# Kernel optimization log

Hardware: AMD Instinct MI355X
Metric: run time of the kernel (lower is better)

The kernel has to match this reference:

```python
import jax, jax.numpy as jnp
import numpy as np

N_NODES = 50000
IN_CH = 128
OUT_CH = 64
HID = 2 * OUT_CH  # 128
N_EDGES = 800000


def _glorot(key, shape):
    fan_in, fan_out = shape[0], shape[-1]
    lim = jnp.sqrt(6.0 / (fan_in + fan_out))
    return jax.random.uniform(key, shape, jnp.float32, -lim, lim)


def setup_inputs() -> dict:
    key = jax.random.key(0)
    ks = jax.random.split(key, 10)
    x = jax.random.normal(ks[0], (N_NODES, IN_CH), jnp.float32)
    edge_index = jax.random.randint(ks[1], (2, N_EDGES), 0, N_NODES, jnp.int32)
    return {
        "x": x,
        "edge_index": edge_index,
        "W1": _glorot(ks[2], (IN_CH, HID)),
        "a_src1": _glorot(ks[3], (HID,)),
        "a_dst1": _glorot(ks[4], (HID,)),
        "b1": jnp.zeros((HID,), jnp.float32),
        "W2": _glorot(ks[5], (HID, OUT_CH)),
        "a_src2": _glorot(ks[6], (OUT_CH,)),
        "a_dst2": _glorot(ks[7], (OUT_CH,)),
        "b2": jnp.zeros((OUT_CH,), jnp.float32),
    }


def _gat_conv(x, src, dst, W, a_src, a_dst, b, n_nodes):
    # Linear transform: [N, F_out]
    h = x @ W
    # Per-node attention halves (heads=1): alpha_i = <h_i, a>
    al_s = h @ a_src  # [N]
    al_d = h @ a_dst  # [N]
    # Edge scores with LeakyReLU(0.2), PyG default negative slope
    e = jax.nn.leaky_relu(al_s[src] + al_d[dst], negative_slope=0.2)
    # Segment softmax over incoming edges of each dst node
    m = jax.ops.segment_max(e, dst, num_segments=n_nodes)
    m = jnp.where(jnp.isfinite(m), m, 0.0)
    ex = jnp.exp(e - m[dst])
    denom = jax.ops.segment_sum(ex, dst, num_segments=n_nodes)
    alpha = ex / (denom[dst] + 1e-16)  # [E]
    # Weighted scatter-add aggregation
    out = jax.ops.segment_sum(h[src] * alpha[:, None], dst, num_segments=n_nodes)
    return out + b


def reference(x, edge_index, W1, a_src1, a_dst1, b1, W2, a_src2, a_dst2, b2):
    n = x.shape[0]
    # add_self_loops=True (PyG GATConv default)
    loops = jnp.arange(n, dtype=edge_index.dtype)
    src = jnp.concatenate([edge_index[0], loops])
    dst = jnp.concatenate([edge_index[1], loops])
    h = _gat_conv(x.astype(jnp.float32), src, dst, W1, a_src1, a_dst1, b1, n)
    h = jax.nn.relu(h)
    return _gat_conv(h, src, dst, W2, a_src2, a_dst2, b2, n)
```

## Files before the change

### kernel.cpp

```cpp
#include <hip/hip_runtime.h>
#include <hip/hip_bf16.h>

#define N_NODES 50000
#define IN_CH 128
#define HID 128
#define OUT_CH 64
#define N_EDGES 800000
#define N_TOT_EDGES (N_EDGES + N_NODES)
#define ET_PAD (N_TOT_EDGES + 3 * N_NODES)
#define MPAD 50048
#define NBN ((N_NODES + 255) / 256)
#define NB_E ((N_EDGES + 255) / 256)
#define NB_ET ((N_TOT_EDGES + 255) / 256)
#define NB_GEMM (MPAD / 64)

typedef float float4v __attribute__((ext_vector_type(4)));
typedef unsigned uint4v __attribute__((ext_vector_type(4)));
typedef __attribute__((ext_vector_type(8))) short bf16x8;
typedef __attribute__((ext_vector_type(4))) float f32x4;

__device__ __forceinline__ unsigned bf16_rne(float f) {
    unsigned u = __float_as_uint(f);
    return (u + 0x7fffu + ((u >> 16) & 1u)) >> 16;
}
__device__ __forceinline__ unsigned pack2(float a, float b) {
    return bf16_rne(a) | (bf16_rne(b) << 16);
}

__global__ __launch_bounds__(256) void k_pre(
        int* __restrict__ cnt,
        const float* __restrict__ W1, unsigned short* __restrict__ Wl1,
        const float* __restrict__ W2, unsigned short* __restrict__ Wl2, int n) {
    const int b = blockIdx.x, t = threadIdx.x;
    if (b < NBN) {
        int i = b * 256 + t;
        if (i < n) cnt[i] = 1;
        return;
    }
    const float* W; unsigned short* Wl; int N, bb;
    if (b < NBN + 8) { W = W1; Wl = Wl1; N = 128; bb = b - NBN; }
    else             { W = W2; Wl = Wl2; N = 64;  bb = b - NBN - 8; }
    const int tg = bb * 256 + t;
    if (tg >= 16 * N) return;
    const int kg = tg / N, col = tg & (N - 1);
    float v[8];
    #pragma unroll
    for (int j = 0; j < 8; ++j) v[j] = W[(size_t)(kg * 8 + j) * N + col];
    uint4 p;
    p.x = pack2(v[0], v[1]); p.y = pack2(v[2], v[3]);
    p.z = pack2(v[4], v[5]); p.w = pack2(v[6], v[7]);
    *(uint4*)&Wl[(size_t)tg * 8] = p;
}


__device__ __forceinline__ void count_body(int b, int t,
        const int* __restrict__ dst_row, int* __restrict__ cnt,
        unsigned short* __restrict__ rank, int e) {
    int i = b * 256 + t;
    if (i < e) {
        int d = __builtin_nontemporal_load(&dst_row[i]);
        rank[i] = (unsigned short)atomicAdd(&cnt[d], 1);
    }
}

template<int N, bool AF32>
__device__ __forceinline__ void gemm_body(int gb, int t,
        const float* __restrict__ Xf, const unsigned short* __restrict__ Xb,
        const unsigned short* __restrict__ Wlg,
        const float* __restrict__ asrc, const float* __restrict__ adst,
        unsigned short* __restrict__ Hb, float* __restrict__ als,
        float* __restrict__ ald, int M, unsigned short* Wl) {
    constexpr int NF = N / 16;
    for (int i = t; i < N * 16; i += 256)
        ((uint4*)Wl)[i] = ((const uint4*)Wlg)[i];
    __syncthreads();

    const int lane = t & 63, w = t >> 6;
    const int rb = gb * 64 + w * 16;
    const int cl = lane & 15, g = lane >> 4;

    f32x4 acc[NF];
    #pragma unroll
    for (int n = 0; n < NF; ++n) acc[n] = (f32x4){0.f, 0.f, 0.f, 0.f};

    const float* Xrow = nullptr;
    const unsigned short* Abase = nullptr;
    if constexpr (AF32) {
        const int arow = (rb + cl < M) ? (rb + cl) : (M - 1);
        Xrow = Xf + (size_t)arow * 128;
    } else {
        Abase = Xb + (size_t)(rb >> 4) * 2048 + cl * 8;
    }

    #pragma unroll
    for (int s = 0; s < 4; ++s) {
        bf16x8 af;
        if constexpr (AF32) {
            const int k0 = (s * 4 + g) * 8;
            float4 a = *(const float4*)&Xrow[k0];
            float4 c = *(const float4*)&Xrow[k0 + 4];
            uint4v uu;
            uu[0] = pack2(a.x, a.y); uu[1] = pack2(a.z, a.w);
            uu[2] = pack2(c.x, c.y); uu[3] = pack2(c.z, c.w);
            af = __builtin_bit_cast(bf16x8, uu);
        } else {
            af = *(const bf16x8*)(Abase + (s * 4 + g) * 128);
        }
        #pragma unroll
        for (int n = 0; n < NF; ++n) {
            bf16x8 bf = *(const bf16x8*)(Wl + ((s * 4 + g) * N + n * 16 + cl) * 8);
            acc[n] = __builtin_amdgcn_mfma_f32_16x16x32_bf16(af, bf, acc[n], 0, 0, 0);
        }
    }

    float asv[NF], adv[NF];
    #pragma unroll
    for (int n = 0; n < NF; ++n) {
        asv[n] = asrc[n * 16 + cl];
        adv[n] = adst[n * 16 + cl];
    }

    #pragma unroll
    for (int r = 0; r < 4; ++r) {
        float ps = 0.f, pd = 0.f;
        #pragma unroll
        for (int n = 0; n < NF; ++n) {
            ps += acc[n][r] * asv[n];
            pd += acc[n][r] * adv[n];
        }
        #pragma unroll
        for (int mask = 1; mask < 16; mask <<= 1) {
            ps += __shfl_xor(ps, mask);
            pd += __shfl_xor(pd, mask);
        }
        const int row = rb + g * 4 + r;
        if (cl == 0 && row < M) { als[row] = ps; ald[row] = pd; }
    }

    #pragma unroll
    for (int r = 0; r < 4; ++r) {
        const int row = rb + g * 4 + r;
        if (row >= M) continue;
        #pragma unroll
        for (int n = 0; n < NF; ++n)
            Hb[(size_t)(n >> 1) * (size_t)M * 32 + (size_t)row * 32
               + (n & 1) * 16 + cl] = (unsigned short)bf16_rne(acc[n][r]);
    }
}

__global__ __launch_bounds__(256) void k_par1(
        const int* __restrict__ ei, int* __restrict__ cnt,
        unsigned short* __restrict__ rank,
        const float* __restrict__ X, const unsigned short* __restrict__ Wl1,
        const float* __restrict__ asrc, const float* __restrict__ adst,
        unsigned short* __restrict__ Hb, float* __restrict__ als,
        float* __restrict__ ald, int M) {
    __shared__ unsigned short Wl[16 * 128 * 8];
    const int b = blockIdx.x, t = threadIdx.x;
    if (b < NB_E) { count_body(b, t, ei + N_EDGES, cnt, rank, N_EDGES); return; }
    gemm_body<HID, true>(b - NB_E, t, X, nullptr, Wl1, asrc, adst, Hb, als, ald, M, Wl);
}


__global__ void k_scan1(const int* __restrict__ cnt, int* __restrict__ off,
                        int* __restrict__ bsum, int n) {
    __shared__ int s[256];
    int t = threadIdx.x;
    int i = blockIdx.x * 256 + t;
    int v = (i < n) ? ((cnt[i] + 3) & ~3) : 0;
    s[t] = v;
    __syncthreads();
    for (int d = 1; d < 256; d <<= 1) {
        int x = (t >= d) ? s[t - d] : 0;
        __syncthreads();
        s[t] += x;
        __syncthreads();
    }
    if (i < n) off[i + 1] = s[t];
    if (t == 255) bsum[blockIdx.x] = s[255];
}

__global__ void k_scan2(int* __restrict__ bsum, int nb) {
    __shared__ int s[256];
    int t = threadIdx.x;
    int v = (t < nb) ? bsum[t] : 0;
    s[t] = v;
    __syncthreads();
    for (int d = 1; d < 256; d <<= 1) {
        int x = (t >= d) ? s[t - d] : 0;
        __syncthreads();
        s[t] += x;
        __syncthreads();
    }
    if (t < nb) bsum[t] = s[t] - v;
}

__global__ void k_scan3(int* __restrict__ off, const int* __restrict__ bsum, int n) {
    int i = blockIdx.x * 256 + threadIdx.x;
    if (i < n) off[i + 1] += bsum[blockIdx.x];
    if (i == 0) off[0] = 0;
}

__global__ void k_fill2(const int* __restrict__ ei, const int* __restrict__ off,
                        const unsigned short* __restrict__ rank,
                        int* __restrict__ csr, int e, int n) {
    int i = blockIdx.x * 256 + threadIdx.x;
    if (i < e) {
        int src = __builtin_nontemporal_load(&ei[i]);
        int dst = __builtin_nontemporal_load(&ei[e + i]);
        csr[off[dst] + rank[i]] = src;
    } else if (i < e + n) {
        int v = i - e;
        csr[off[v]] = v;
    }
}

__global__ __launch_bounds__(256) void gemm_mfma64(
        const unsigned short* __restrict__ Xb, const unsigned short* __restrict__ Wlg,
        const float* __restrict__ asrc, const float* __restrict__ adst,
        unsigned short* __restrict__ Hb, float* __restrict__ als,
        float* __restrict__ ald, int M) {
    __shared__ unsigned short Wl[16 * 64 * 8];
    gemm_body<OUT_CH, false>(blockIdx.x, threadIdx.x, nullptr, Xb, Wlg,
                             asrc, adst, Hb, als, ald, M, Wl);
}

template<bool PADZ>
__global__ __launch_bounds__(256) void k_edgew(
        const float* __restrict__ als, const float* __restrict__ ald,
        const int* __restrict__ off, const int* __restrict__ cnt,
        const int* __restrict__ csr,
        unsigned* __restrict__ ew, float* __restrict__ invden, int n) {
    const int fl = threadIdx.x & 15;
    const int v = blockIdx.x * 16 + (threadIdx.x >> 4);
    if (v >= n) return;
    const int start = off[v], end = start + cnt[v];
    const float aldv = ald[v];
    float s = 0.f;
    for (int j = start + fl; j < end; j += 16) {
        int src = __builtin_nontemporal_load(&csr[j]);
        float e = als[src] + aldv;
        e = e > 0.f ? e : 0.2f * e;
        unsigned r = bf16_rne(__expf(e));
        ew[j] = ((unsigned)src << 16) | r;
        s += __uint_as_float(r << 16);
    }
    if (PADZ) {
        const int pend = off[v + 1];
        for (int j = end + fl; j < pend; j += 16) ew[j] = 0;
    }
    #pragma unroll
    for (int d = 1; d < 16; d <<= 1) s += __shfl_xor(s, d);
    if (fl == 0) invden[v] = 1.f / (s + 1e-16f);
}

template<int F, bool RELU, bool PACKOUT>
__global__ __launch_bounds__(256) void k_spmm_b(
        const unsigned short* __restrict__ Hb, const unsigned* __restrict__ ew,
        const float* __restrict__ invden, const float* __restrict__ bias,
        const int* __restrict__ off, void* __restrict__ outv, int n) {
    constexpr int NCH = F / 32;
    const int chunk = blockIdx.x % NCH;
    const int v = (blockIdx.x / NCH) * 64 + (threadIdx.x >> 2);
    if (v >= n) return;
    const int q = threadIdx.x & 3;
    const int start = off[v], end = off[v + 1];
    const unsigned short* __restrict__ Hch = Hb + (size_t)chunk * (size_t)n * 32 + q * 8;

    float a0[8] = {}, a1[8] = {}, a2[8] = {}, a3[8] = {};

    #define GATB(E, A)                                                   \
        {                                                                \
            float w_ = __uint_as_float((E) << 16);                       \
            uint4 h_ = *(const uint4*)&Hch[(size_t)((E) >> 16) * 32];    \
            A[0] += w_ * __uint_as_float(h_.x << 16);                    \
            A[1] += w_ * __uint_as_float(h_.x & 0xffff0000u);            \
            A[2] += w_ * __uint_as_float(h_.y << 16);                    \
            A[3] += w_ * __uint_as_float(h_.y & 0xffff0000u);            \
            A[4] += w_ * __uint_as_float(h_.z << 16);                    \
            A[5] += w_ * __uint_as_float(h_.z & 0xffff0000u);            \
            A[6] += w_ * __uint_as_float(h_.w << 16);                    \
            A[7] += w_ * __uint_as_float(h_.w & 0xffff0000u);            \
        }
    #define GATB4(Q) GATB((Q).x, a0) GATB((Q).y, a1) GATB((Q).z, a2) GATB((Q).w, a3)

    int j = start;
    for (; j + 4 < end; j += 8) {
        uint4 eA = *(const uint4*)&ew[j];
        uint4 eB = *(const uint4*)&ew[j + 4];
        GATB4(eA)
        GATB4(eB)
    }
    if (j < end) {
        uint4 eA = *(const uint4*)&ew[j];
        GATB4(eA)
    }
    #undef GATB4
    #undef GATB

    const float inv = invden[v];
    const float* __restrict__ bp = bias + chunk * 32 + q * 8;
    float s[8];
    #pragma unroll
    for (int i = 0; i < 8; ++i) {
        s[i] = (a0[i] + a1[i] + a2[i] + a3[i]) * inv + bp[i];
        if (RELU) s[i] = fmaxf(s[i], 0.f);
    }

    if (PACKOUT) {
        unsigned short* Xb2 = (unsigned short*)outv;
        const int kg = chunk * 4 + q;
        uint4v p;
        p[0] = pack2(s[0], s[1]); p[1] = pack2(s[2], s[3]);
        p[2] = pack2(s[4], s[5]); p[3] = pack2(s[6], s[7]);
        __builtin_nontemporal_store(p,
            (uint4v*)&Xb2[(size_t)(v >> 4) * 2048 + kg * 128 + (v & 15) * 8]);
    } else {
        float* out = (float*)outv;
        float4v o0, o1;
        o0[0] = s[0]; o0[1] = s[1]; o0[2] = s[2]; o0[3] = s[3];
        o1[0] = s[4]; o1[1] = s[5]; o1[2] = s[6]; o1[3] = s[7];
        float* op = out + (size_t)v * F + chunk * 32 + q * 8;
        __builtin_nontemporal_store(o0, (float4v*)op);
        __builtin_nontemporal_store(o1, (float4v*)(op + 4));
    }
}


extern "C" void kernel_launch(void* const* d_in, const int* in_sizes, int n_in,
                              void* d_out, int out_size, void* d_ws, size_t ws_size,
                              hipStream_t stream) {
    const float* x     = (const float*)d_in[0];
    const int*   ei    = (const int*)d_in[1];
    const float* W1    = (const float*)d_in[2];
    const float* as1   = (const float*)d_in[3];
    const float* ad1   = (const float*)d_in[4];
    const float* b1    = (const float*)d_in[5];
    const float* W2    = (const float*)d_in[6];
    const float* as2   = (const float*)d_in[7];
    const float* ad2   = (const float*)d_in[8];
    const float* b2    = (const float*)d_in[9];
    float* out = (float*)d_out;

    const int Nn = N_NODES;

    char* ws = (char*)d_ws;
    size_t o = 0;
    auto carve = [&](size_t bytes) { char* p = ws + o; o = (o + bytes + 255) & ~(size_t)255; return p; };
    int*            off  = (int*)carve((Nn + 1) * sizeof(int));
    int*            cnt  = (int*)carve(Nn * sizeof(int));
    int*            bsum = (int*)carve(256 * sizeof(int));
    unsigned short* rank = (unsigned short*)carve((size_t)N_EDGES * sizeof(unsigned short));
    int*            csr  = (int*)carve((size_t)ET_PAD * sizeof(int));
    unsigned*       ew   = (unsigned*)carve((size_t)ET_PAD * sizeof(unsigned));
    unsigned short* h1b  = (unsigned short*)carve((size_t)Nn * HID * sizeof(unsigned short));
    unsigned short* h2b  = (unsigned short*)carve((size_t)Nn * OUT_CH * sizeof(unsigned short));
    unsigned short* Xb2  = (unsigned short*)carve((size_t)MPAD * 128 * sizeof(unsigned short));
    unsigned short* Wl1  = (unsigned short*)carve(16 * 128 * 8 * sizeof(unsigned short));
    unsigned short* Wl2  = (unsigned short*)carve(16 * 64 * 8 * sizeof(unsigned short));
    float*          als  = (float*)carve(Nn * sizeof(float));
    float*          ald  = (float*)carve(Nn * sizeof(float));
    float*          invd = (float*)carve(Nn * sizeof(float));

    k_pre<<<NBN + 12, 256, 0, stream>>>(cnt, W1, Wl1, W2, Wl2, Nn);

    k_par1<<<NB_E + NB_GEMM, 256, 0, stream>>>(
        ei, cnt, rank, x, Wl1, as1, ad1, h1b, als, ald, Nn);

    k_scan1<<<NBN, 256, 0, stream>>>(cnt, off, bsum, Nn);
    k_scan2<<<1, 256, 0, stream>>>(bsum, NBN);
    k_scan3<<<NBN, 256, 0, stream>>>(off, bsum, Nn);

    k_fill2<<<NB_ET, 256, 0, stream>>>(ei, off, rank, csr, N_EDGES, Nn);

    const int nbEW  = (Nn + 15) / 16;
    const int nbN64 = (Nn + 63) / 64;

    k_edgew<true><<<nbEW, 256, 0, stream>>>(als, ald, off, cnt, csr, ew, invd, Nn);
    k_spmm_b<HID, true, true><<<nbN64 * (HID / 32), 256, 0, stream>>>(
        h1b, ew, invd, b1, off, Xb2, Nn);

    gemm_mfma64<<<NB_GEMM, 256, 0, stream>>>(
        Xb2, Wl2, as2, ad2, h2b, als, ald, Nn);
    k_edgew<false><<<nbEW, 256, 0, stream>>>(als, ald, off, cnt, csr, ew, invd, Nn);
    k_spmm_b<OUT_CH, false, false><<<nbN64 * (OUT_CH / 32), 256, 0, stream>>>(
        h2b, ew, invd, b2, off, out, Nn);
}
```

Before: 162.7 us.

## Split degree-count atomics into eight sub-histograms to cut contention

The per-destination degree counter becomes eight counter arrays, chosen by block index modulo eight, so concurrent atomics on the same node spread across separate addresses. The scan kernel then sums the eight partial counts into a total, stores per-copy prefix offsets as 16-bit values, and the CSR fill adds the matching offset to each edge's rank. This aims to reduce atomic serialization in the counting pass. In exchange it zeroes eight times as much counter memory and adds reads of the partial counts and prefix offsets in the scan and fill kernels.

```diff
diff --git a/kernel.cpp b/kernel.cpp
--- a/kernel.cpp
+++ b/kernel.cpp
@@ -13,6 +13,7 @@
 #define NB_E ((N_EDGES + 255) / 256)
 #define NB_ET ((N_TOT_EDGES + 255) / 256)
 #define NB_GEMM (MPAD / 64)
+#define NB8 ((8 * N_NODES + 255) / 256)
 
 typedef float float4v __attribute__((ext_vector_type(4)));
 typedef unsigned uint4v __attribute__((ext_vector_type(4)));
@@ -28,18 +29,18 @@
 }
 
 __global__ __launch_bounds__(256) void k_pre(
-        int* __restrict__ cnt,
+        int* __restrict__ cnt8,
         const float* __restrict__ W1, unsigned short* __restrict__ Wl1,
-        const float* __restrict__ W2, unsigned short* __restrict__ Wl2, int n) {
+        const float* __restrict__ W2, unsigned short* __restrict__ Wl2) {
     const int b = blockIdx.x, t = threadIdx.x;
-    if (b < NBN) {
+    if (b < NB8) {
         int i = b * 256 + t;
-        if (i < n) cnt[i] = 1;
+        if (i < 8 * N_NODES) cnt8[i] = 0;
         return;
     }
     const float* W; unsigned short* Wl; int N, bb;
-    if (b < NBN + 8) { W = W1; Wl = Wl1; N = 128; bb = b - NBN; }
-    else             { W = W2; Wl = Wl2; N = 64;  bb = b - NBN - 8; }
+    if (b < NB8 + 8) { W = W1; Wl = Wl1; N = 128; bb = b - NB8; }
+    else             { W = W2; Wl = Wl2; N = 64;  bb = b - NB8 - 8; }
     const int tg = bb * 256 + t;
     if (tg >= 16 * N) return;
     const int kg = tg / N, col = tg & (N - 1);
@@ -54,12 +55,13 @@
 
 
 __device__ __forceinline__ void count_body(int b, int t,
-        const int* __restrict__ dst_row, int* __restrict__ cnt,
+        const int* __restrict__ dst_row, int* __restrict__ cnt8,
         unsigned short* __restrict__ rank, int e) {
     int i = b * 256 + t;
     if (i < e) {
         int d = __builtin_nontemporal_load(&dst_row[i]);
-        rank[i] = (unsigned short)atomicAdd(&cnt[d], 1);
+        int c = b & 7;
+        rank[i] = (unsigned short)atomicAdd(&cnt8[c * N_NODES + d], 1);
     }
 }
 
@@ -149,7 +151,7 @@
 }
 
 __global__ __launch_bounds__(256) void k_par1(
-        const int* __restrict__ ei, int* __restrict__ cnt,
+        const int* __restrict__ ei, int* __restrict__ cnt8,
         unsigned short* __restrict__ rank,
         const float* __restrict__ X, const unsigned short* __restrict__ Wl1,
         const float* __restrict__ asrc, const float* __restrict__ adst,
@@ -157,18 +159,35 @@
         float* __restrict__ ald, int M) {
     __shared__ unsigned short Wl[16 * 128 * 8];
     const int b = blockIdx.x, t = threadIdx.x;
-    if (b < NB_E) { count_body(b, t, ei + N_EDGES, cnt, rank, N_EDGES); return; }
+    if (b < NB_E) { count_body(b, t, ei + N_EDGES, cnt8, rank, N_EDGES); return; }
     gemm_body<HID, true>(b - NB_E, t, X, nullptr, Wl1, asrc, adst, Hb, als, ald, M, Wl);
 }
 
-
-__global__ void k_scan1(const int* __restrict__ cnt, int* __restrict__ off,
-                        int* __restrict__ bsum, int n) {
+__global__ void k_scan1(const int* __restrict__ cnt8, int* __restrict__ cntT,
+                        unsigned short* __restrict__ pcoff,
+                        int* __restrict__ off, int* __restrict__ bsum, int n) {
     __shared__ int s[256];
     int t = threadIdx.x;
     int i = blockIdx.x * 256 + t;
-    int v = (i < n) ? ((cnt[i] + 3) & ~3) : 0;
-    s[t] = v;
+    int padded = 0;
+    if (i < n) {
+        int pc = 1;
+        unsigned short po[8];
+        #pragma unroll
+        for (int c = 0; c < 8; ++c) {
+            po[c] = (unsigned short)pc;
+            pc += cnt8[c * n + i];
+        }
+        cntT[i] = pc;
+        uint4 p;
+        p.x = (unsigned)po[0] | ((unsigned)po[1] << 16);
+        p.y = (unsigned)po[2] | ((unsigned)po[3] << 16);
+        p.z = (unsigned)po[4] | ((unsigned)po[5] << 16);
+        p.w = (unsigned)po[6] | ((unsigned)po[7] << 16);
+        *(uint4*)&pcoff[(size_t)i * 8] = p;
+        padded = (pc + 3) & ~3;
+    }
+    s[t] = padded;
     __syncthreads();
     for (int d = 1; d < 256; d <<= 1) {
         int x = (t >= d) ? s[t - d] : 0;
@@ -203,12 +222,15 @@
 
 __global__ void k_fill2(const int* __restrict__ ei, const int* __restrict__ off,
                         const unsigned short* __restrict__ rank,
+                        const unsigned short* __restrict__ pcoff,
                         int* __restrict__ csr, int e, int n) {
     int i = blockIdx.x * 256 + threadIdx.x;
     if (i < e) {
         int src = __builtin_nontemporal_load(&ei[i]);
         int dst = __builtin_nontemporal_load(&ei[e + i]);
-        csr[off[dst] + rank[i]] = src;
+        int c = (i >> 8) & 7;
+        int pos = off[dst] + (int)pcoff[(size_t)dst * 8 + c] + (int)rank[i];
+        csr[pos] = src;
     } else if (i < e + n) {
         int v = i - e;
         csr[off[v]] = v;
@@ -228,13 +250,13 @@
 template<bool PADZ>
 __global__ __launch_bounds__(256) void k_edgew(
         const float* __restrict__ als, const float* __restrict__ ald,
-        const int* __restrict__ off, const int* __restrict__ cnt,
+        const int* __restrict__ off, const int* __restrict__ cntT,
         const int* __restrict__ csr,
         unsigned* __restrict__ ew, float* __restrict__ invden, int n) {
     const int fl = threadIdx.x & 15;
     const int v = blockIdx.x * 16 + (threadIdx.x >> 4);
     if (v >= n) return;
-    const int start = off[v], end = start + cnt[v];
+    const int start = off[v], end = start + cntT[v];
     const float aldv = ald[v];
     float s = 0.f;
     for (int j = start + fl; j < end; j += 16) {
@@ -348,9 +370,11 @@
     size_t o = 0;
     auto carve = [&](size_t bytes) { char* p = ws + o; o = (o + bytes + 255) & ~(size_t)255; return p; };
     int*            off  = (int*)carve((Nn + 1) * sizeof(int));
-    int*            cnt  = (int*)carve(Nn * sizeof(int));
+    int*            cnt8 = (int*)carve((size_t)8 * Nn * sizeof(int));
+    int*            cntT = (int*)carve(Nn * sizeof(int));
     int*            bsum = (int*)carve(256 * sizeof(int));
     unsigned short* rank = (unsigned short*)carve((size_t)N_EDGES * sizeof(unsigned short));
+    unsigned short* pcoff= (unsigned short*)carve((size_t)Nn * 8 * sizeof(unsigned short));
     int*            csr  = (int*)carve((size_t)ET_PAD * sizeof(int));
     unsigned*       ew   = (unsigned*)carve((size_t)ET_PAD * sizeof(unsigned));
     unsigned short* h1b  = (unsigned short*)carve((size_t)Nn * HID * sizeof(unsigned short));
@@ -362,27 +386,27 @@
     float*          ald  = (float*)carve(Nn * sizeof(float));
     float*          invd = (float*)carve(Nn * sizeof(float));
 
-    k_pre<<<NBN + 12, 256, 0, stream>>>(cnt, W1, Wl1, W2, Wl2, Nn);
+    k_pre<<<NB8 + 12, 256, 0, stream>>>(cnt8, W1, Wl1, W2, Wl2);
 
     k_par1<<<NB_E + NB_GEMM, 256, 0, stream>>>(
-        ei, cnt, rank, x, Wl1, as1, ad1, h1b, als, ald, Nn);
-
-    k_scan1<<<NBN, 256, 0, stream>>>(cnt, off, bsum, Nn);
+        ei, cnt8, rank, x, Wl1, as1, ad1, h1b, als, ald, Nn);
+
+    k_scan1<<<NBN, 256, 0, stream>>>(cnt8, cntT, pcoff, off, bsum, Nn);
     k_scan2<<<1, 256, 0, stream>>>(bsum, NBN);
     k_scan3<<<NBN, 256, 0, stream>>>(off, bsum, Nn);
 
-    k_fill2<<<NB_ET, 256, 0, stream>>>(ei, off, rank, csr, N_EDGES, Nn);
+    k_fill2<<<NB_ET, 256, 0, stream>>>(ei, off, rank, pcoff, csr, N_EDGES, Nn);
 
     const int nbEW  = (Nn + 15) / 16;
     const int nbN64 = (Nn + 63) / 64;
 
-    k_edgew<true><<<nbEW, 256, 0, stream>>>(als, ald, off, cnt, csr, ew, invd, Nn);
+    k_edgew<true><<<nbEW, 256, 0, stream>>>(als, ald, off, cntT, csr, ew, invd, Nn);
     k_spmm_b<HID, true, true><<<nbN64 * (HID / 32), 256, 0, stream>>>(
         h1b, ew, invd, b1, off, Xb2, Nn);
 
     gemm_mfma64<<<NB_GEMM, 256, 0, stream>>>(
         Xb2, Wl2, as2, ad2, h2b, als, ald, Nn);
-    k_edgew<false><<<nbEW, 256, 0, stream>>>(als, ald, off, cnt, csr, ew, invd, Nn);
+    k_edgew<false><<<nbEW, 256, 0, stream>>>(als, ald, off, cntT, csr, ew, invd, Nn);
     k_spmm_b<OUT_CH, false, false><<<nbN64 * (OUT_CH / 32), 256, 0, stream>>>(
         h2b, ew, invd, b2, off, out, Nn);
 }
```

After: 163.9 us. No clear change (+0.7%).
